# Performance work log

Hardware: AMD Instinct MI355X
Metric: run time of the kernel (lower is better)

Reference implementation:

```python
import jax, jax.numpy as jnp
import numpy as np

D_MODEL = 2048
N_HEADS = 16
D_HEAD = 128
D_LATENT = 512


def setup_inputs() -> dict:
    key = jax.random.key(0)
    ks = jax.random.split(key, 5)
    s = lambda fan_in: 1.0 / np.sqrt(fan_in)
    x = jax.random.normal(ks[0], (2, 2048, D_MODEL), dtype=jnp.float32)
    # nn.Linear weights stored as [out, in]; we keep [in, out] for x @ W
    W_q = jax.random.uniform(ks[1], (D_MODEL, N_HEADS * D_HEAD), jnp.float32, -s(D_MODEL), s(D_MODEL))
    W_kv_down = jax.random.uniform(ks[2], (D_MODEL, D_LATENT), jnp.float32, -s(D_MODEL), s(D_MODEL))
    W_kv_up = jax.random.uniform(ks[3], (D_LATENT, N_HEADS * D_HEAD), jnp.float32, -s(D_LATENT), s(D_LATENT))
    W_o = jax.random.uniform(ks[4], (N_HEADS * D_HEAD, D_MODEL), jnp.float32, -s(N_HEADS * D_HEAD), s(N_HEADS * D_HEAD))
    return {"x": x, "W_q": W_q, "W_kv_down": W_kv_down, "W_kv_up": W_kv_up, "W_o": W_o}


def reference(x, W_q, W_kv_down, W_kv_up, W_o):
    B, S, _ = x.shape
    # q: [B, H, S, Dh]
    q = (x @ W_q).reshape(B, S, N_HEADS, D_HEAD).transpose(0, 2, 1, 3)
    # latent compression then up-projection; shared K = V
    latent = x @ W_kv_down                      # [B, S, Dl]
    kv = (latent @ W_kv_up).reshape(B, S, N_HEADS, D_HEAD).transpose(0, 2, 1, 3)
    scale = 1.0 / np.sqrt(D_HEAD).astype(np.float32)
    scores = jnp.einsum('bhqd,bhkd->bhqk', q, kv) * scale  # [B,H,S,S]
    probs = jax.nn.softmax(scores, axis=-1)
    out = jnp.einsum('bhqk,bhkd->bhqd', probs, kv)          # [B,H,S,Dh]
    out = out.transpose(0, 2, 1, 3).reshape(B, S, N_HEADS * D_HEAD)
    return out @ W_o
```

## Files before the change

kernel.cpp:

```cpp
#include <hip/hip_runtime.h>

typedef __attribute__((ext_vector_type(8))) __bf16 bf16x8;
typedef __attribute__((ext_vector_type(4))) float f32x4;
typedef __attribute__((ext_vector_type(8))) unsigned short u16x8;
typedef __attribute__((ext_vector_type(4))) unsigned short u16x4;
typedef __attribute__((ext_vector_type(2))) unsigned int u32x2;
typedef __attribute__((ext_vector_type(4))) unsigned int u32x4;

#define MFMA16(a, b, c) __builtin_amdgcn_mfma_f32_16x16x32_bf16((a), (b), (c), 0, 0, 0)

__device__ __forceinline__ unsigned short f2bf(float f) {
    unsigned int u = __float_as_uint(f);
    unsigned int r = (u + 0x7FFFu + ((u >> 16) & 1u)) >> 16;
    return (unsigned short)r;
}

__device__ __forceinline__ u32x2 plswap32(unsigned int x, unsigned int y) {
#if __has_builtin(__builtin_amdgcn_permlane32_swap)
    return __builtin_amdgcn_permlane32_swap(x, y, false, false);
#else
    asm volatile("s_nop 1\n\tv_permlane32_swap_b32 %0, %1" : "+v"(x), "+v"(y));
    u32x2 r = {x, y};
    return r;
#endif
}
__device__ __forceinline__ u32x2 plswap16(unsigned int x, unsigned int y) {
#if __has_builtin(__builtin_amdgcn_permlane16_swap)
    return __builtin_amdgcn_permlane16_swap(x, y, false, false);
#else
    asm volatile("s_nop 1\n\tv_permlane16_swap_b32 %0, %1" : "+v"(x), "+v"(y));
    u32x2 r = {x, y};
    return r;
#endif
}

__device__ __forceinline__ float quad_reduce(float v) {
    u32x2 a = plswap32(__float_as_uint(v), __float_as_uint(v));
    v = __uint_as_float(a.x) + __uint_as_float(a.y);
    u32x2 b = plswap16(__float_as_uint(v), __float_as_uint(v));
    return __uint_as_float(b.x) + __uint_as_float(b.y);
}

__device__ __forceinline__ void transpose_tile(const float* __restrict__ in,
                                               unsigned short* __restrict__ out,
                                               int R, int C, int bx, int by) {
    __shared__ float tile[32][33];
    const int tx = threadIdx.x & 31, ty = threadIdx.x >> 5;
    const int c0 = bx * 32, r0 = by * 32;
#pragma unroll
    for (int i = 0; i < 4; ++i)
        tile[ty + i * 8][tx] = in[(size_t)(r0 + ty + i * 8) * C + c0 + tx];
    __syncthreads();
#pragma unroll
    for (int i = 0; i < 4; ++i)
        out[(size_t)(c0 + ty + i * 8) * R + r0 + tx] = f2bf(tile[tx][ty + i * 8]);
}

__global__ __launch_bounds__(256) void k_prep(const float* __restrict__ x,
                                              const float* __restrict__ Wq,
                                              const float* __restrict__ Wkvd,
                                              const float* __restrict__ Wkvu,
                                              const float* __restrict__ Wo,
                                              unsigned short* __restrict__ xb,
                                              unsigned short* __restrict__ Wcat_t,
                                              unsigned short* __restrict__ Wkvu_t,
                                              unsigned short* __restrict__ Wo_t) {
    const int i = blockIdx.x;
    if (i < 8192) {
        const int idx = i * 256 + threadIdx.x;
        const float4 v = ((const float4*)x)[idx];
        u16x4 o = { f2bf(v.x), f2bf(v.y), f2bf(v.z), f2bf(v.w) };
        ((u16x4*)xb)[idx] = o;
    } else if (i < 12288) {
        const int j = i - 8192;
        transpose_tile(Wq, Wcat_t, 2048, 2048, j & 63, j >> 6);
    } else if (i < 13312) {
        const int j = i - 12288;
        transpose_tile(Wkvd, Wcat_t + 2048 * 2048, 2048, 512, j & 15, j >> 4);
    } else if (i < 14336) {
        const int j = i - 13312;
        transpose_tile(Wkvu, Wkvu_t, 512, 2048, j & 63, j >> 6);
    } else {
        const int j = i - 14336;
        transpose_tile(Wo, Wo_t, 2048, 2048, j & 63, j >> 6);
    }
}

template <int OUT_MODE>
__global__ __launch_bounds__(256) void k_gemm_bt(const unsigned short* __restrict__ A,
                                                 const unsigned short* __restrict__ B,
                                                 void* __restrict__ Cv,
                                                 unsigned short* __restrict__ Ct,
                                                 int M, int N, int K, float alpha) {
    __shared__ alignas(16) unsigned short As[2 * 128 * 32];
    __shared__ alignas(16) unsigned short Bs[2 * 128 * 32];
    const int tid = threadIdx.x;
    const int wave = tid >> 6;
    const int lane = tid & 63;
    const int l16 = lane & 15;
    const int quad = lane >> 4;
    const int bm = blockIdx.x * 128;
    const int bn = blockIdx.y * 128;
    const int wm = (wave >> 1) * 64;
    const int wn = (wave & 1) * 64;

    const f32x4 fzero = {0.f, 0.f, 0.f, 0.f};
    f32x4 acc[4][4];
#pragma unroll
    for (int i = 0; i < 4; ++i)
#pragma unroll
        for (int j = 0; j < 4; ++j) acc[i][j] = fzero;

    auto AsL = (__attribute__((address_space(3))) unsigned short*)As;
    auto BsL = (__attribute__((address_space(3))) unsigned short*)Bs;

    const int c0 = wave * 128 + lane;

    auto stage = [&](int kt32) {
        const int boff = (kt32 & 1) * (128 * 32);
        const int kt = kt32 * 32;
#pragma unroll
        for (int j = 0; j < 2; ++j) {
            const int c = c0 + j * 64;
            __builtin_amdgcn_global_load_lds(
                (const __attribute__((address_space(1))) void*)(A + (size_t)(bm + (c >> 2)) * K + kt + (c & 3) * 8),
                (__attribute__((address_space(3))) void*)(AsL + boff + c * 8), 16, 0, 0);
            __builtin_amdgcn_global_load_lds(
                (const __attribute__((address_space(1))) void*)(B + (size_t)(bn + (c >> 2)) * K + kt + (c & 3) * 8),
                (__attribute__((address_space(3))) void*)(BsL + boff + c * 8), 16, 0, 0);
        }
    };

    const int nk = K >> 5;
    stage(0);
    for (int kt32 = 0; kt32 < nk; ++kt32) {
        __syncthreads();
        if (kt32 + 1 < nk) stage(kt32 + 1);
        const unsigned short* Ab = As + (kt32 & 1) * (128 * 32);
        const unsigned short* Bb = Bs + (kt32 & 1) * (128 * 32);

        bf16x8 af[4], bfr[4];
#pragma unroll
        for (int mt = 0; mt < 4; ++mt)
            af[mt] = *(const bf16x8*)(Ab + (wm + mt * 16 + l16) * 32 + quad * 8);
#pragma unroll
        for (int nt = 0; nt < 4; ++nt)
            bfr[nt] = *(const bf16x8*)(Bb + (wn + nt * 16 + l16) * 32 + quad * 8);
#pragma unroll
        for (int mt = 0; mt < 4; ++mt)
#pragma unroll
            for (int nt = 0; nt < 4; ++nt)
                acc[mt][nt] = MFMA16(af[mt], bfr[nt], acc[mt][nt]);
    }

#pragma unroll
    for (int mt = 0; mt < 4; ++mt)
#pragma unroll
        for (int nt = 0; nt < 4; ++nt) {
            const int row0 = bm + wm + mt * 16 + quad * 4;
            const int col = bn + wn + nt * 16 + l16;
            u16x4 pk;
#pragma unroll
            for (int r = 0; r < 4; ++r) {
                const float v0 = acc[mt][nt][r];
                if (OUT_MODE == 0) {
                    ((float*)Cv)[(size_t)(row0 + r) * N + col] = v0 * alpha;
                } else if (OUT_MODE == 3) {
                    if (col < 2048)
                        ((unsigned short*)Cv)[(size_t)(row0 + r) * 2048 + col] = f2bf(v0 * alpha);
                    else
                        Ct[(size_t)(row0 + r) * 512 + (col - 2048)] = f2bf(v0);
                } else {
                    const unsigned short b = f2bf(v0 * alpha);
                    ((unsigned short*)Cv)[(size_t)(row0 + r) * N + col] = b;
                    pk[r] = b;
                }
            }
            if (OUT_MODE == 2) {
                const size_t ti =
                    ((size_t)((row0 >> 11) * (N >> 7) + (col >> 7)) * 128 + (col & 127)) * 2048 +
                    (row0 & 2047);
                *(u16x4*)(Ct + ti) = pk;
            }
        }
}

__global__ __launch_bounds__(256, 2) void k_attn(const unsigned short* __restrict__ Q,
                                                 const unsigned short* __restrict__ KV,
                                                 const unsigned short* __restrict__ KVT,
                                                 unsigned short* __restrict__ O) {
    __shared__ alignas(16) unsigned short Ks[2 * 64 * 128];
    __shared__ alignas(16) unsigned short Vt[2 * 128 * 64];

    const int tid = threadIdx.x;
    const int wave = tid >> 6, lane = tid & 63;
    const int l16 = lane & 15, quad = lane >> 4;
    const int l8 = l16 & 7;
    const int lid = blockIdx.x + (blockIdx.y << 4);
    const int wid = ((lid & 7) << 6) + (lid >> 3);
    const int qt = wid & 15;
    const int bh = wid >> 4;
    const size_t tokbase = (size_t)(bh >> 4) * 2048;
    const int hcol = (bh & 15) * 128;
    const unsigned short* kvt_head = KVT + (size_t)bh * (128 * 2048);

    bf16x8 qf[2][4];
    const int qrow0 = qt * 128 + wave * 32;
#pragma unroll
    for (int nt = 0; nt < 2; ++nt) {
        const unsigned short* qp =
            Q + (tokbase + qrow0 + nt * 16 + l16) * 2048 + hcol + quad * 8;
#pragma unroll
        for (int kd = 0; kd < 4; ++kd) qf[nt][kd] = *(const bf16x8*)(qp + kd * 32);
    }

    const f32x4 fzero = {0.f, 0.f, 0.f, 0.f};
    f32x4 o_acc[8][2];
#pragma unroll
    for (int dt = 0; dt < 8; ++dt)
#pragma unroll
        for (int nt = 0; nt < 2; ++nt) o_acc[dt][nt] = fzero;
    float l_i[2] = {0.f, 0.f};

    const int krow = tid >> 4, kchunk = tid & 15;
    const int vrow = tid >> 3, vchunk = tid & 7;

    u16x8 kR[4], vR[4];
    auto load_tile = [&](int kt) {
#pragma unroll
        for (int p = 0; p < 4; ++p) {
            kR[p] = *(const u16x8*)(KV + (tokbase + kt * 64 + p * 16 + krow) * 2048 +
                                    hcol + kchunk * 8);
            vR[p] = *(const u16x8*)(kvt_head + (size_t)(p * 32 + vrow) * 2048 + kt * 64 +
                                    vchunk * 8);
        }
    };
    auto store_tile = [&](int kt) {
        unsigned short* Kb = Ks + (kt & 1) * (64 * 128);
        unsigned short* Vb = Vt + (kt & 1) * (128 * 64);
#pragma unroll
        for (int p = 0; p < 4; ++p) {
            const int r = p * 16 + krow;
            const int swk = (kchunk & 8) | ((kchunk & 7) ^ (r & 7));
            *(u16x8*)(Kb + r * 128 + swk * 8) = kR[p];
            const int d = p * 32 + vrow;
            const int swv = vchunk ^ (d & 7);
            *(u16x8*)(Vb + d * 64 + swv * 8) = vR[p];
        }
    };

    load_tile(0);
    store_tile(0);
    load_tile(1);

    for (int kt = 0; kt < 32; ++kt) {
        __syncthreads();
        if (kt < 31) {
            store_tile(kt + 1);
            if (kt < 30) load_tile(kt + 2);
        }
        const unsigned short* Kb = Ks + (kt & 1) * (64 * 128);
        const unsigned short* Vb = Vt + (kt & 1) * (128 * 64);

        f32x4 st[4][2];
#pragma unroll
        for (int mt = 0; mt < 4; ++mt)
#pragma unroll
            for (int nt = 0; nt < 2; ++nt) st[mt][nt] = fzero;
#pragma unroll
        for (int kd = 0; kd < 4; ++kd)
#pragma unroll
            for (int mt = 0; mt < 4; ++mt) {
                const int c = kd * 4 + quad;
                const int sw = (c & 8) | ((c & 7) ^ l8);
                const bf16x8 kf = *(const bf16x8*)(Kb + (mt * 16 + l16) * 128 + sw * 8);
                st[mt][0] = MFMA16(kf, qf[0][kd], st[mt][0]);
                st[mt][1] = MFMA16(kf, qf[1][kd], st[mt][1]);
            }

        bf16x8 pfr[2][2];
#pragma unroll
        for (int nt = 0; nt < 2; ++nt) {
            float p[4][4];
            float rs = 0.f;
#pragma unroll
            for (int mt = 0; mt < 4; ++mt)
#pragma unroll
                for (int r = 0; r < 4; ++r) {
                    p[mt][r] = __expf(st[mt][nt][r]);
                    rs += p[mt][r];
                }
            l_i[nt] += quad_reduce(rs);
#pragma unroll
            for (int s = 0; s < 2; ++s) {
                unsigned int aw0, aw1, bw0, bw1;
                asm("v_cvt_pk_bf16_f32 %0, %1, %2" : "=v"(aw0) : "v"(p[2 * s][0]), "v"(p[2 * s][1]));
                asm("v_cvt_pk_bf16_f32 %0, %1, %2" : "=v"(aw1) : "v"(p[2 * s][2]), "v"(p[2 * s][3]));
                asm("v_cvt_pk_bf16_f32 %0, %1, %2" : "=v"(bw0) : "v"(p[2 * s + 1][0]), "v"(p[2 * s + 1][1]));
                asm("v_cvt_pk_bf16_f32 %0, %1, %2" : "=v"(bw1) : "v"(p[2 * s + 1][2]), "v"(p[2 * s + 1][3]));
                const u32x2 e0 = plswap32(aw0, bw0);
                const u32x2 e1 = plswap32(aw1, bw1);
                const u32x2 f0 = plswap16(e0.x, e0.y);
                const u32x2 f1 = plswap16(e1.x, e1.y);
                const u32x4 w = {f0.x, f1.x, f0.y, f1.y};
                pfr[s][nt] = __builtin_bit_cast(bf16x8, w);
            }
        }

#pragma unroll
        for (int s = 0; s < 2; ++s) {
            const int sw = ((s * 4 + quad) ^ l8) * 8;
#pragma unroll
            for (int dt = 0; dt < 8; ++dt) {
                const bf16x8 vf = *(const bf16x8*)(Vb + (dt * 16 + l16) * 64 + sw);
                o_acc[dt][0] = MFMA16(vf, pfr[s][0], o_acc[dt][0]);
                o_acc[dt][1] = MFMA16(vf, pfr[s][1], o_acc[dt][1]);
            }
        }
    }

#pragma unroll
    for (int nt = 0; nt < 2; ++nt) {
        const float inv = 1.0f / l_i[nt];
        unsigned short* dst = O + (tokbase + qrow0 + nt * 16 + l16) * 2048 + hcol;
#pragma unroll
        for (int dt = 0; dt < 8; ++dt) {
            u16x4 pk;
#pragma unroll
            for (int r = 0; r < 4; ++r) pk[r] = f2bf(o_acc[dt][nt][r] * inv);
            *(u16x4*)(dst + dt * 16 + quad * 4) = pk;
        }
    }
}

extern "C" void kernel_launch(void* const* d_in, const int* in_sizes, int n_in,
                              void* d_out, int out_size, void* d_ws, size_t ws_size,
                              hipStream_t stream) {
    const float* x = (const float*)d_in[0];
    const float* W_q = (const float*)d_in[1];
    const float* W_kvd = (const float*)d_in[2];
    const float* W_kvu = (const float*)d_in[3];
    const float* W_o = (const float*)d_in[4];

    char* w = (char*)d_ws;
    unsigned short* xb = (unsigned short*)(w);
    unsigned short* kvT = xb;
    unsigned short* qb = (unsigned short*)(w + (size_t)16 * 1024 * 1024);
    unsigned short* kvb = (unsigned short*)(w + (size_t)32 * 1024 * 1024);
    unsigned short* Wo_t = (unsigned short*)(w + (size_t)48 * 1024 * 1024);
    unsigned short* Wcat_t = (unsigned short*)(w + (size_t)56 * 1024 * 1024);
    unsigned short* Wkvu_t = (unsigned short*)(w + (size_t)66 * 1024 * 1024);
    unsigned short* lat = (unsigned short*)(w + (size_t)68 * 1024 * 1024);

    k_prep<<<18432, 256, 0, stream>>>(x, W_q, W_kvd, W_kvu, W_o, xb, Wcat_t, Wkvu_t, Wo_t);

    k_gemm_bt<3><<<dim3(32, 20), 256, 0, stream>>>(xb, Wcat_t, qb, lat, 4096, 2560, 2048,
                                                   0.08838834764831845f);
    k_gemm_bt<2><<<dim3(32, 16), 256, 0, stream>>>(lat, Wkvu_t, kvb, kvT, 4096, 2048, 512,
                                                   1.0f);
    k_attn<<<dim3(16, 32), 256, 0, stream>>>(qb, kvb, kvT, qb);
    k_gemm_bt<0><<<dim3(32, 16), 256, 0, stream>>>(qb, Wo_t, d_out, nullptr, 4096, 2048, 2048,
                                                   1.0f);
}
```

Measured before the change: 309.4 us.

## Read V from K tile via LDS transpose reads, drop separate KV transpose

After: 316.2 us. +2.2%, slower.

```diff
diff --git a/kernel.cpp b/kernel.cpp
--- a/kernel.cpp
+++ b/kernel.cpp
@@ -6,6 +6,7 @@
 typedef __attribute__((ext_vector_type(4))) unsigned short u16x4;
 typedef __attribute__((ext_vector_type(2))) unsigned int u32x2;
 typedef __attribute__((ext_vector_type(4))) unsigned int u32x4;
+typedef __attribute__((ext_vector_type(4))) short s16x4;
 
 #define MFMA16(a, b, c) __builtin_amdgcn_mfma_f32_16x16x32_bf16((a), (b), (c), 0, 0, 0)
 
@@ -39,6 +40,19 @@
     v = __uint_as_float(a.x) + __uint_as_float(a.y);
     u32x2 b = plswap16(__float_as_uint(v), __float_as_uint(v));
     return __uint_as_float(b.x) + __uint_as_float(b.y);
+}
+
+__device__ __forceinline__ s16x4 tr16(const __attribute__((address_space(3))) unsigned short* p) {
+#if __has_builtin(__builtin_amdgcn_ds_read_tr16_b64)
+    return __builtin_amdgcn_ds_read_tr16_b64(
+        (__attribute__((address_space(3))) s16x4*)p);
+#else
+    s16x4 d;
+    asm volatile("ds_read_b64_tr_b16 %0, %1\n\ts_waitcnt lgkmcnt(0)"
+                 : "=v"(d) : "v"(p) : "memory");
+    __builtin_amdgcn_sched_barrier(0);
+    return d;
+#endif
 }
 
 __device__ __forceinline__ void transpose_tile(const float* __restrict__ in,
@@ -159,7 +173,6 @@
         for (int nt = 0; nt < 4; ++nt) {
             const int row0 = bm + wm + mt * 16 + quad * 4;
             const int col = bn + wn + nt * 16 + l16;
-            u16x4 pk;
 #pragma unroll
             for (int r = 0; r < 4; ++r) {
                 const float v0 = acc[mt][nt][r];
@@ -171,26 +184,16 @@
                     else
                         Ct[(size_t)(row0 + r) * 512 + (col - 2048)] = f2bf(v0);
                 } else {
-                    const unsigned short b = f2bf(v0 * alpha);
-                    ((unsigned short*)Cv)[(size_t)(row0 + r) * N + col] = b;
-                    pk[r] = b;
+                    ((unsigned short*)Cv)[(size_t)(row0 + r) * N + col] = f2bf(v0 * alpha);
                 }
-            }
-            if (OUT_MODE == 2) {
-                const size_t ti =
-                    ((size_t)((row0 >> 11) * (N >> 7) + (col >> 7)) * 128 + (col & 127)) * 2048 +
-                    (row0 & 2047);
-                *(u16x4*)(Ct + ti) = pk;
             }
         }
 }
 
 __global__ __launch_bounds__(256, 2) void k_attn(const unsigned short* __restrict__ Q,
                                                  const unsigned short* __restrict__ KV,
-                                                 const unsigned short* __restrict__ KVT,
                                                  unsigned short* __restrict__ O) {
     __shared__ alignas(16) unsigned short Ks[2 * 64 * 128];
-    __shared__ alignas(16) unsigned short Vt[2 * 128 * 64];
 
     const int tid = threadIdx.x;
     const int wave = tid >> 6, lane = tid & 63;
@@ -202,7 +205,6 @@
     const int bh = wid >> 4;
     const size_t tokbase = (size_t)(bh >> 4) * 2048;
     const int hcol = (bh & 15) * 128;
-    const unsigned short* kvt_head = KVT + (size_t)bh * (128 * 2048);
 
     bf16x8 qf[2][4];
     const int qrow0 = qt * 128 + wave * 32;
@@ -223,31 +225,40 @@
     float l_i[2] = {0.f, 0.f};
 
     const int krow = tid >> 4, kchunk = tid & 15;
-    const int vrow = tid >> 3, vchunk = tid & 7;
-
-    u16x8 kR[4], vR[4];
+
+    u16x8 kR[4];
     auto load_tile = [&](int kt) {
 #pragma unroll
-        for (int p = 0; p < 4; ++p) {
+        for (int p = 0; p < 4; ++p)
             kR[p] = *(const u16x8*)(KV + (tokbase + kt * 64 + p * 16 + krow) * 2048 +
                                     hcol + kchunk * 8);
-            vR[p] = *(const u16x8*)(kvt_head + (size_t)(p * 32 + vrow) * 2048 + kt * 64 +
-                                    vchunk * 8);
-        }
     };
     auto store_tile = [&](int kt) {
         unsigned short* Kb = Ks + (kt & 1) * (64 * 128);
-        unsigned short* Vb = Vt + (kt & 1) * (128 * 64);
 #pragma unroll
         for (int p = 0; p < 4; ++p) {
             const int r = p * 16 + krow;
             const int swk = (kchunk & 8) | ((kchunk & 7) ^ (r & 7));
             *(u16x8*)(Kb + r * 128 + swk * 8) = kR[p];
-            const int d = p * 32 + vrow;
-            const int swv = vchunk ^ (d & 7);
-            *(u16x8*)(Vb + d * 64 + swv * 8) = vR[p];
         }
     };
+
+    int toff[8][2];
+    {
+        const int rb = quad * 8 + (l16 >> 2);
+        const int e = (l16 & 3) >> 1;
+        const int dlow = (l16 & 1) * 4;
+#pragma unroll
+        for (int dt = 0; dt < 8; ++dt)
+#pragma unroll
+            for (int h = 0; h < 2; ++h) {
+                const int kr = rb + h * 4;
+                const int dc = dt * 2 + e;
+                const int sw = (dc & 8) | ((dc & 7) ^ (kr & 7));
+                toff[dt][h] = kr * 128 + sw * 8 + dlow;
+            }
+    }
+    auto KsL = (const __attribute__((address_space(3))) unsigned short*)Ks;
 
     load_tile(0);
     store_tile(0);
@@ -260,13 +271,14 @@
             if (kt < 30) load_tile(kt + 2);
         }
         const unsigned short* Kb = Ks + (kt & 1) * (64 * 128);
-        const unsigned short* Vb = Vt + (kt & 1) * (128 * 64);
+        const int bufoff = (kt & 1) * (64 * 128);
 
         f32x4 st[4][2];
 #pragma unroll
         for (int mt = 0; mt < 4; ++mt)
 #pragma unroll
             for (int nt = 0; nt < 2; ++nt) st[mt][nt] = fzero;
+        __builtin_amdgcn_s_setprio(1);
 #pragma unroll
         for (int kd = 0; kd < 4; ++kd)
 #pragma unroll
@@ -277,6 +289,7 @@
                 st[mt][0] = MFMA16(kf, qf[0][kd], st[mt][0]);
                 st[mt][1] = MFMA16(kf, qf[1][kd], st[mt][1]);
             }
+        __builtin_amdgcn_s_setprio(0);
 
         bf16x8 pfr[2][2];
 #pragma unroll
@@ -307,16 +320,20 @@
             }
         }
 
+        __builtin_amdgcn_s_setprio(1);
 #pragma unroll
         for (int s = 0; s < 2; ++s) {
-            const int sw = ((s * 4 + quad) ^ l8) * 8;
+            const int sbase = bufoff + s * 4096;
 #pragma unroll
             for (int dt = 0; dt < 8; ++dt) {
-                const bf16x8 vf = *(const bf16x8*)(Vb + (dt * 16 + l16) * 64 + sw);
-                o_acc[dt][0] = MFMA16(vf, pfr[s][0], o_acc[dt][0]);
-                o_acc[dt][1] = MFMA16(vf, pfr[s][1], o_acc[dt][1]);
-            }
-        }
+                union { s16x4 q[2]; bf16x8 b; } u;
+                u.q[0] = tr16(KsL + sbase + toff[dt][0]);
+                u.q[1] = tr16(KsL + sbase + toff[dt][1]);
+                o_acc[dt][0] = MFMA16(u.b, pfr[s][0], o_acc[dt][0]);
+                o_acc[dt][1] = MFMA16(u.b, pfr[s][1], o_acc[dt][1]);
+            }
+        }
+        __builtin_amdgcn_s_setprio(0);
     }
 
 #pragma unroll
@@ -344,7 +361,6 @@
 
     char* w = (char*)d_ws;
     unsigned short* xb = (unsigned short*)(w);
-    unsigned short* kvT = xb;
     unsigned short* qb = (unsigned short*)(w + (size_t)16 * 1024 * 1024);
     unsigned short* kvb = (unsigned short*)(w + (size_t)32 * 1024 * 1024);
     unsigned short* Wo_t = (unsigned short*)(w + (size_t)48 * 1024 * 1024);
@@ -356,9 +372,9 @@
 
     k_gemm_bt<3><<<dim3(32, 20), 256, 0, stream>>>(xb, Wcat_t, qb, lat, 4096, 2560, 2048,
                                                    0.08838834764831845f);
-    k_gemm_bt<2><<<dim3(32, 16), 256, 0, stream>>>(lat, Wkvu_t, kvb, kvT, 4096, 2048, 512,
+    k_gemm_bt<1><<<dim3(32, 16), 256, 0, stream>>>(lat, Wkvu_t, kvb, nullptr, 4096, 2048, 512,
                                                    1.0f);
-    k_attn<<<dim3(16, 32), 256, 0, stream>>>(qb, kvb, kvT, qb);
+    k_attn<<<dim3(16, 32), 256, 0, stream>>>(qb, kvb, qb);
     k_gemm_bt<0><<<dim3(32, 16), 256, 0, stream>>>(qb, Wo_t, d_out, nullptr, 4096, 2048, 2048,
                                                    1.0f);
 }
```

## Use 8 waves of 16 query rows each in attention and raise MFMA priority

Applied to the files above, without the earlier changes.

After: 326.9 us. +5.7%, slower.

```diff
diff --git a/kernel.cpp b/kernel.cpp
--- a/kernel.cpp
+++ b/kernel.cpp
@@ -185,7 +185,7 @@
         }
 }
 
-__global__ __launch_bounds__(256, 2) void k_attn(const unsigned short* __restrict__ Q,
+__global__ __launch_bounds__(512, 4) void k_attn(const unsigned short* __restrict__ Q,
                                                  const unsigned short* __restrict__ KV,
                                                  const unsigned short* __restrict__ KVT,
                                                  unsigned short* __restrict__ O) {
@@ -204,47 +204,44 @@
     const int hcol = (bh & 15) * 128;
     const unsigned short* kvt_head = KVT + (size_t)bh * (128 * 2048);
 
-    bf16x8 qf[2][4];
-    const int qrow0 = qt * 128 + wave * 32;
-#pragma unroll
-    for (int nt = 0; nt < 2; ++nt) {
-        const unsigned short* qp =
-            Q + (tokbase + qrow0 + nt * 16 + l16) * 2048 + hcol + quad * 8;
-#pragma unroll
-        for (int kd = 0; kd < 4; ++kd) qf[nt][kd] = *(const bf16x8*)(qp + kd * 32);
+    bf16x8 qf[4];
+    const int qrow0 = qt * 128 + wave * 16;
+    {
+        const unsigned short* qp = Q + (tokbase + qrow0 + l16) * 2048 + hcol + quad * 8;
+#pragma unroll
+        for (int kd = 0; kd < 4; ++kd) qf[kd] = *(const bf16x8*)(qp + kd * 32);
     }
 
     const f32x4 fzero = {0.f, 0.f, 0.f, 0.f};
-    f32x4 o_acc[8][2];
-#pragma unroll
-    for (int dt = 0; dt < 8; ++dt)
-#pragma unroll
-        for (int nt = 0; nt < 2; ++nt) o_acc[dt][nt] = fzero;
-    float l_i[2] = {0.f, 0.f};
-
-    const int krow = tid >> 4, kchunk = tid & 15;
-    const int vrow = tid >> 3, vchunk = tid & 7;
-
-    u16x8 kR[4], vR[4];
+    f32x4 o_acc[8];
+#pragma unroll
+    for (int dt = 0; dt < 8; ++dt) o_acc[dt] = fzero;
+    float l_i = 0.f;
+
+    u16x8 kR[2], vR[2];
     auto load_tile = [&](int kt) {
 #pragma unroll
-        for (int p = 0; p < 4; ++p) {
-            kR[p] = *(const u16x8*)(KV + (tokbase + kt * 64 + p * 16 + krow) * 2048 +
-                                    hcol + kchunk * 8);
-            vR[p] = *(const u16x8*)(kvt_head + (size_t)(p * 32 + vrow) * 2048 + kt * 64 +
-                                    vchunk * 8);
+        for (int p = 0; p < 2; ++p) {
+            const int ks = p * 512 + tid;
+            kR[p] = *(const u16x8*)(KV + (tokbase + kt * 64 + (ks >> 4)) * 2048 +
+                                    hcol + (ks & 15) * 8);
+            const int vs = p * 512 + tid;
+            vR[p] = *(const u16x8*)(kvt_head + (size_t)(vs >> 3) * 2048 + kt * 64 +
+                                    (vs & 7) * 8);
         }
     };
     auto store_tile = [&](int kt) {
         unsigned short* Kb = Ks + (kt & 1) * (64 * 128);
         unsigned short* Vb = Vt + (kt & 1) * (128 * 64);
 #pragma unroll
-        for (int p = 0; p < 4; ++p) {
-            const int r = p * 16 + krow;
-            const int swk = (kchunk & 8) | ((kchunk & 7) ^ (r & 7));
+        for (int p = 0; p < 2; ++p) {
+            const int ks = p * 512 + tid;
+            const int r = ks >> 4, kc = ks & 15;
+            const int swk = (kc & 8) | ((kc & 7) ^ (r & 7));
             *(u16x8*)(Kb + r * 128 + swk * 8) = kR[p];
-            const int d = p * 32 + vrow;
-            const int swv = vchunk ^ (d & 7);
+            const int vs = p * 512 + tid;
+            const int d = vs >> 3, vc = vs & 7;
+            const int swv = vc ^ (d & 7);
             *(u16x8*)(Vb + d * 64 + swv * 8) = vR[p];
         }
     };
@@ -262,11 +259,10 @@
         const unsigned short* Kb = Ks + (kt & 1) * (64 * 128);
         const unsigned short* Vb = Vt + (kt & 1) * (128 * 64);
 
-        f32x4 st[4][2];
-#pragma unroll
-        for (int mt = 0; mt < 4; ++mt)
-#pragma unroll
-            for (int nt = 0; nt < 2; ++nt) st[mt][nt] = fzero;
+        f32x4 st[4];
+#pragma unroll
+        for (int mt = 0; mt < 4; ++mt) st[mt] = fzero;
+        __builtin_amdgcn_s_setprio(1);
 #pragma unroll
         for (int kd = 0; kd < 4; ++kd)
 #pragma unroll
@@ -274,23 +270,22 @@
                 const int c = kd * 4 + quad;
                 const int sw = (c & 8) | ((c & 7) ^ l8);
                 const bf16x8 kf = *(const bf16x8*)(Kb + (mt * 16 + l16) * 128 + sw * 8);
-                st[mt][0] = MFMA16(kf, qf[0][kd], st[mt][0]);
-                st[mt][1] = MFMA16(kf, qf[1][kd], st[mt][1]);
-            }
-
-        bf16x8 pfr[2][2];
-#pragma unroll
-        for (int nt = 0; nt < 2; ++nt) {
+                st[mt] = MFMA16(kf, qf[kd], st[mt]);
+            }
+        __builtin_amdgcn_s_setprio(0);
+
+        bf16x8 pfr[2];
+        {
             float p[4][4];
             float rs = 0.f;
 #pragma unroll
             for (int mt = 0; mt < 4; ++mt)
 #pragma unroll
                 for (int r = 0; r < 4; ++r) {
-                    p[mt][r] = __expf(st[mt][nt][r]);
+                    p[mt][r] = __expf(st[mt][r]);
                     rs += p[mt][r];
                 }
-            l_i[nt] += quad_reduce(rs);
+            l_i += quad_reduce(rs);
 #pragma unroll
             for (int s = 0; s < 2; ++s) {
                 unsigned int aw0, aw1, bw0, bw1;
@@ -303,31 +298,31 @@
                 const u32x2 f0 = plswap16(e0.x, e0.y);
                 const u32x2 f1 = plswap16(e1.x, e1.y);
                 const u32x4 w = {f0.x, f1.x, f0.y, f1.y};
-                pfr[s][nt] = __builtin_bit_cast(bf16x8, w);
-            }
-        }
-
+                pfr[s] = __builtin_bit_cast(bf16x8, w);
+            }
+        }
+
+        __builtin_amdgcn_s_setprio(1);
 #pragma unroll
         for (int s = 0; s < 2; ++s) {
             const int sw = ((s * 4 + quad) ^ l8) * 8;
 #pragma unroll
             for (int dt = 0; dt < 8; ++dt) {
                 const bf16x8 vf = *(const bf16x8*)(Vb + (dt * 16 + l16) * 64 + sw);
-                o_acc[dt][0] = MFMA16(vf, pfr[s][0], o_acc[dt][0]);
-                o_acc[dt][1] = MFMA16(vf, pfr[s][1], o_acc[dt][1]);
-            }
-        }
-    }
-
-#pragma unroll
-    for (int nt = 0; nt < 2; ++nt) {
-        const float inv = 1.0f / l_i[nt];
-        unsigned short* dst = O + (tokbase + qrow0 + nt * 16 + l16) * 2048 + hcol;
+                o_acc[dt] = MFMA16(vf, pfr[s], o_acc[dt]);
+            }
+        }
+        __builtin_amdgcn_s_setprio(0);
+    }
+
+    {
+        const float inv = 1.0f / l_i;
+        unsigned short* dst = O + (tokbase + qrow0 + l16) * 2048 + hcol;
 #pragma unroll
         for (int dt = 0; dt < 8; ++dt) {
             u16x4 pk;
 #pragma unroll
-            for (int r = 0; r < 4; ++r) pk[r] = f2bf(o_acc[dt][nt][r] * inv);
+            for (int r = 0; r < 4; ++r) pk[r] = f2bf(o_acc[dt][r] * inv);
             *(u16x4*)(dst + dt * 16 + quad * 4) = pk;
         }
     }
@@ -358,7 +353,7 @@
                                                    0.08838834764831845f);
     k_gemm_bt<2><<<dim3(32, 16), 256, 0, stream>>>(lat, Wkvu_t, kvb, kvT, 4096, 2048, 512,
                                                    1.0f);
-    k_attn<<<dim3(16, 32), 256, 0, stream>>>(qb, kvb, kvT, qb);
+    k_attn<<<dim3(16, 32), 512, 0, stream>>>(qb, kvb, kvT, qb);
     k_gemm_bt<0><<<dim3(32, 16), 256, 0, stream>>>(qb, Wo_t, d_out, nullptr, 4096, 2048, 2048,
                                                    1.0f);
 }
```
